# Performance work log

Hardware: AMD Instinct MI355X
Metric: run time of the kernel (lower is better)

Reference implementation:

```python
import jax, jax.numpy as jnp
import numpy as np
from jax import lax

NUM_TAGS = 9
HIDDEN = 768
BATCH = 64
SEQ = 512


def setup_inputs() -> dict:
    key = jax.random.key(0)
    ks = jax.random.split(key, 6)
    hidden = jax.random.normal(ks[0], (BATCH, SEQ, HIDDEN), dtype=jnp.float32)
    labels = jax.random.randint(ks[1], (BATCH, SEQ), 0, NUM_TAGS)  # all >= 0 -> full mask
    weight = jax.random.normal(ks[2], (NUM_TAGS, HIDDEN), dtype=jnp.float32) * 0.02
    bias = jnp.zeros((NUM_TAGS,), dtype=jnp.float32)
    start_transitions = jax.random.normal(ks[3], (NUM_TAGS,), dtype=jnp.float32) * 0.1
    end_transitions = jax.random.normal(ks[4], (NUM_TAGS,), dtype=jnp.float32) * 0.1
    transitions = jax.random.normal(ks[5], (NUM_TAGS, NUM_TAGS), dtype=jnp.float32) * 0.1
    return dict(hidden=hidden, labels=labels, weight=weight, bias=bias,
                start_transitions=start_transitions, end_transitions=end_transitions,
                transitions=transitions)


def _crf_log_likelihood(emissions, tags, mask, start_t, end_t, trans):
    """pytorch-crf log-likelihood, reduction='sum'.
    emissions [B,L,T] float, tags [B,L] int, mask [B,L] bool."""
    # --- numerator: score of the gold path ---
    tag0 = tags[:, 0]
    score0 = start_t[tag0] + jnp.take_along_axis(emissions[:, 0], tag0[:, None], axis=1)[:, 0]

    def num_step(carry, inp):
        score, prev = carry
        em, tg, m = inp  # em [B,T], tg [B], m [B]
        s = trans[prev, tg] + jnp.take_along_axis(em, tg[:, None], axis=1)[:, 0]
        score = score + jnp.where(m, s, jnp.zeros_like(s))
        prev = jnp.where(m, tg, prev)
        return (score, prev), None

    (num_score, last_tag), _ = lax.scan(
        num_step, (score0, tag0),
        (emissions[:, 1:].swapaxes(0, 1), tags[:, 1:].T, mask[:, 1:].T))
    numerator = num_score + end_t[last_tag]

    # --- denominator: forward algorithm (log-sum-exp recurrence) ---
    alpha0 = start_t[None, :] + emissions[:, 0]  # [B,T]

    def den_step(alpha, inp):
        em, m = inp  # em [B,T], m [B]
        nxt = jax.nn.logsumexp(alpha[:, :, None] + trans[None], axis=1) + em
        alpha = jnp.where(m[:, None], nxt, alpha)
        return alpha, None

    alpha, _ = lax.scan(den_step, alpha0,
                        (emissions[:, 1:].swapaxes(0, 1), mask[:, 1:].T))
    denominator = jax.nn.logsumexp(alpha + end_t[None, :], axis=1)

    return jnp.sum(numerator - denominator)


def _viterbi_decode(emissions, mask, start_t, end_t, trans):
    """Max-plus DP + backtrack. Returns padded [B,L] int32 best tag sequence."""
    B, L, T = emissions.shape
    score0 = start_t[None, :] + emissions[:, 0]  # [B,T]
    identity = jnp.arange(T, dtype=jnp.int32)[None, :]  # identity backpointer for masked steps

    def fwd_step(score, inp):
        em, m = inp  # em [B,T], m [B]
        br = score[:, :, None] + trans[None]  # [B,T_prev,T_cur]
        idx = jnp.argmax(br, axis=1).astype(jnp.int32)  # [B,T]
        nxt = jnp.max(br, axis=1) + em
        score = jnp.where(m[:, None], nxt, score)
        idx = jnp.where(m[:, None], idx, identity)
        return score, idx

    final, hist = lax.scan(fwd_step, score0,
                           (emissions[:, 1:].swapaxes(0, 1), mask[:, 1:].T))
    last_tag = jnp.argmax(final + end_t[None, :], axis=1).astype(jnp.int32)  # [B]

    def back_step(tag, idx):  # idx [B,T] backpointers for this position
        prev = jnp.take_along_axis(idx, tag[:, None], axis=1)[:, 0]
        return prev, tag

    first_tag, tags_rev = lax.scan(back_step, last_tag, hist, reverse=True)
    tags = jnp.concatenate([first_tag[None, :], tags_rev], axis=0).T  # [B,L]
    return tags * mask.astype(jnp.int32)


def reference(hidden, labels, weight, bias, start_transitions, end_transitions, transitions):
    mask_full = labels >= 0
    h = hidden[:, 1:-1, :]                       # drop [CLS]/[SEP] positions
    tags = labels[:, 1:-1] * mask_full[:, 1:-1]  # zero out padded labels
    mask = mask_full[:, 1:-1]
    # dropout is identity in eval mode
    emissions = jnp.einsum('blh,th->blt', h, weight) + bias  # [B,L,T]
    llh = _crf_log_likelihood(emissions, tags, mask,
                              start_transitions, end_transitions, transitions)
    tag_seqs = _viterbi_decode(emissions, mask,
                               start_transitions, end_transitions, transitions)
    return -llh, tag_seqs.astype(jnp.float32)
```

## Files before the change

kernel.cpp:

```cpp
#include <hip/hip_runtime.h>
#include <stdint.h>

#define NB 64
#define SEQL 512
#define L 510
#define T 9
#define H 768
#define EMS 12
#define LN2 0.6931471805599453f

__device__ __forceinline__ float rl(float v, int l) {
  return __uint_as_float(__builtin_amdgcn_readlane(__float_as_uint(v), l));
}

__global__ __launch_bounds__(256) void ka_kernel(
    const float* __restrict__ hidden, const float* __restrict__ weight,
    const float* __restrict__ bias, const float* __restrict__ trans,
    float* __restrict__ em, float* __restrict__ PdLn, float* __restrict__ Mv,
    float* __restrict__ out) {
  __shared__ float4 wl[1728];
  __shared__ float s_em[33 * 12];
  __shared__ float s_ee[33 * 12];
  const int tid = threadIdx.x;
  const int w = blockIdx.x;
  const int b = w >> 4, s = w & 15;
  const int nt = (s == 15) ? 29 : 32;
  const int l0 = 32 * s + 1;
  const int off0 = (s == 0) ? 1 : 0;
  const int nrows = nt + off0;
  const int lstart = l0 - off0;

  const float4* w4 = (const float4*)weight;
  for (int k = tid; k < 1728; k += 256) wl[k] = w4[k];
  if (w == 0 && tid == 0) out[0] = 0.f;
  __syncthreads();

  const int lane = tid & 63, wv = tid >> 6;
  float bs[9];
#pragma unroll
  for (int t = 0; t < 9; ++t) bs[t] = bias[t];

  for (int r = wv; r < nrows; r += 4) {
    const float4* h4 = (const float4*)(hidden + ((size_t)(b * SEQL + lstart + r + 1)) * H);
    float4 h0 = h4[lane], h1 = h4[lane + 64], h2 = h4[lane + 128];
    float acc[9];
#pragma unroll
    for (int t = 0; t < 9; ++t) acc[t] = 0.f;
#pragma unroll
    for (int t = 0; t < 9; ++t) {
      float4 wa = wl[t * 192 + lane];
      float4 wb = wl[t * 192 + lane + 64];
      float4 wc = wl[t * 192 + lane + 128];
      acc[t] = fmaf(h0.x, wa.x, fmaf(h0.y, wa.y, fmaf(h0.z, wa.z, fmaf(h0.w, wa.w, acc[t]))));
      acc[t] = fmaf(h1.x, wb.x, fmaf(h1.y, wb.y, fmaf(h1.z, wb.z, fmaf(h1.w, wb.w, acc[t]))));
      acc[t] = fmaf(h2.x, wc.x, fmaf(h2.y, wc.y, fmaf(h2.z, wc.z, fmaf(h2.w, wc.w, acc[t]))));
    }
#pragma unroll
    for (int off = 32; off; off >>= 1) {
#pragma unroll
      for (int t = 0; t < 9; ++t) acc[t] += __shfl_xor(acc[t], off);
    }
    if (lane == 0) {
      float* eo = em + ((size_t)(b * L + lstart + r)) * EMS;
#pragma unroll
      for (int t = 0; t < 9; ++t) {
        float v = acc[t] + bs[t];
        s_em[r * 12 + t] = v;
        s_ee[r * 12 + t] = __expf(v);
        eo[t] = v;
      }
    }
  }
  __syncthreads();

  if (tid < 64) {
    const int i9 = lane < 9 ? lane : 8;
    float E[81];
#pragma unroll
    for (int k = 0; k < 81; ++k) E[k] = __expf(trans[k]);
    const float* ee0 = s_ee + off0 * 12;
    float R[9];
#pragma unroll
    for (int j = 0; j < 9; ++j) R[j] = E[i9 * 9 + j] * ee0[j];
    int iexp = 0;
    for (int t = 1; t < nt; ++t) {
      const float* e = ee0 + t * 12;
      float4 ea = *(const float4*)e;
      float4 eb = *(const float4*)(e + 4);
      float e8 = e[8];
      float Rn[9];
#pragma unroll
      for (int j = 0; j < 9; ++j) {
        float a = R[0] * E[0 * 9 + j];
#pragma unroll
        for (int k = 1; k < 9; ++k) a = fmaf(R[k], E[k * 9 + j], a);
        Rn[j] = a;
      }
      R[0] = Rn[0] * ea.x; R[1] = Rn[1] * ea.y; R[2] = Rn[2] * ea.z;
      R[3] = Rn[3] * ea.w; R[4] = Rn[4] * eb.x; R[5] = Rn[5] * eb.y;
      R[6] = Rn[6] * eb.z; R[7] = Rn[7] * eb.w; R[8] = Rn[8] * e8;
      if ((t & 3) == 0) {
        float mx = R[0];
#pragma unroll
        for (int j = 1; j < 9; ++j) mx = fmaxf(mx, R[j]);
        int ex = (int)((__float_as_uint(mx) >> 23) & 0xff) - 127;
        iexp += ex;
        float sc = __uint_as_float((uint32_t)(127 - ex) << 23);
#pragma unroll
        for (int j = 0; j < 9; ++j) R[j] *= sc;
      }
    }
    if (lane < 9) {
      float ls = (float)iexp * LN2;
#pragma unroll
      for (int j = 0; j < 9; ++j)
        PdLn[(size_t)w * 81 + j * 9 + lane] = __logf(R[j]) + ls;
    }
  } else if (tid < 128) {
    const int i9 = lane < 9 ? lane : 8;
    float t_[81];
#pragma unroll
    for (int k = 0; k < 81; ++k) t_[k] = trans[k];
    const float* e0 = s_em + off0 * 12;
    float V[9];
#pragma unroll
    for (int j = 0; j < 9; ++j) V[j] = t_[i9 * 9 + j] + e0[j];
    for (int t = 1; t < nt; ++t) {
      const float* e = e0 + t * 12;
      float4 ea = *(const float4*)e;
      float4 eb = *(const float4*)(e + 4);
      float e8 = e[8];
      float ex[9] = {ea.x, ea.y, ea.z, ea.w, eb.x, eb.y, eb.z, eb.w, e8};
      float Vn[9];
#pragma unroll
      for (int j = 0; j < 9; ++j) {
        float m = V[0] + t_[0 * 9 + j];
#pragma unroll
        for (int k = 1; k < 9; ++k) m = fmaxf(m, V[k] + t_[k * 9 + j]);
        Vn[j] = m + ex[j];
      }
#pragma unroll
      for (int j = 0; j < 9; ++j) V[j] = Vn[j];
    }
    if (lane < 9) {
#pragma unroll
      for (int j = 0; j < 9; ++j)
        Mv[(size_t)w * 81 + j * 9 + lane] = V[j];
    }
  }
}

__global__ __launch_bounds__(256) void kb_kernel(
    const float* __restrict__ em, const int* __restrict__ labels,
    const float* __restrict__ PdLn, const float* __restrict__ Mv,
    const float* __restrict__ start_t, const float* __restrict__ end_t,
    const float* __restrict__ trans, float* __restrict__ out) {
  __shared__ float s_pd[1296];
  __shared__ float s_mv[1296];
  __shared__ float s_A[153];
  __shared__ float s_t[81];
  __shared__ float s_np[4];
  __shared__ int s_lab[L];
  __shared__ unsigned char s_ch[32];
  __shared__ uint32_t s_bp[32 * 16 * 2];
  const int b = blockIdx.x;
  const int tid = threadIdx.x;
  for (int k = tid; k < 1296; k += 256) {
    s_pd[k] = PdLn[(size_t)b * 1296 + k];
    s_mv[k] = Mv[(size_t)b * 1296 + k];
  }
  for (int k = tid; k < 81; k += 256) s_t[k] = trans[k];
  for (int k = tid; k < L; k += 256) s_lab[k] = labels[b * SEQL + 1 + k];
  __syncthreads();

  float part = 0.f;
  for (int l = tid; l < L; l += 256) {
    int tg = s_lab[l];
    float e = em[((size_t)(b * L + l)) * EMS + tg];
    if (l == 0) part += start_t[tg] + e;
    else part += s_t[s_lab[l - 1] * 9 + tg] + e;
    if (l == L - 1) part += end_t[tg];
  }
#pragma unroll
  for (int off = 32; off; off >>= 1) part += __shfl_xor(part, off);
  if ((tid & 63) == 0) s_np[tid >> 6] = part;
  __syncthreads();

  if (tid < 64) {
    const int lane = tid;
    const int jj = lane < 9 ? lane : 8;

    float D = start_t[jj] + em[(size_t)b * L * EMS + jj];
    for (int s = 0; s < 16; ++s) {
      const float* col = &s_pd[s * 81 + jj * 9];
      float v0 = rl(D, 0) + col[0], v1 = rl(D, 1) + col[1], v2 = rl(D, 2) + col[2];
      float v3 = rl(D, 3) + col[3], v4 = rl(D, 4) + col[4], v5 = rl(D, 5) + col[5];
      float v6 = rl(D, 6) + col[6], v7 = rl(D, 7) + col[7], v8 = rl(D, 8) + col[8];
      float mx = fmaxf(fmaxf(fmaxf(fmaxf(v0, v1), fmaxf(v2, v3)),
                             fmaxf(fmaxf(v4, v5), fmaxf(v6, v7))), v8);
      float sum = __expf(v0 - mx) + __expf(v1 - mx) + __expf(v2 - mx) +
                  __expf(v3 - mx) + __expf(v4 - mx) + __expf(v5 - mx) +
                  __expf(v6 - mx) + __expf(v7 - mx) + __expf(v8 - mx);
      D = mx + __logf(sum);
    }
    float fe = D + end_t[jj];
    float w0 = rl(fe, 0), w1 = rl(fe, 1), w2 = rl(fe, 2), w3 = rl(fe, 3);
    float w4 = rl(fe, 4), w5 = rl(fe, 5), w6 = rl(fe, 6), w7 = rl(fe, 7), w8 = rl(fe, 8);
    float mx = fmaxf(fmaxf(fmaxf(fmaxf(w0, w1), fmaxf(w2, w3)),
                           fmaxf(fmaxf(w4, w5), fmaxf(w6, w7))), w8);
    float den = mx + __logf(__expf(w0 - mx) + __expf(w1 - mx) + __expf(w2 - mx) +
                            __expf(w3 - mx) + __expf(w4 - mx) + __expf(w5 - mx) +
                            __expf(w6 - mx) + __expf(w7 - mx) + __expf(w8 - mx));
    if (lane == 0)
      atomicAdd(out, den - (s_np[0] + s_np[1] + s_np[2] + s_np[3]));

    float A = start_t[jj] + em[(size_t)b * L * EMS + jj];
    if (lane < 9) s_A[lane] = A;
    for (int s = 0; s < 16; ++s) {
      const float* col = &s_mv[s * 81 + jj * 9];
      float u0 = rl(A, 0) + col[0], u1 = rl(A, 1) + col[1], u2 = rl(A, 2) + col[2];
      float u3 = rl(A, 3) + col[3], u4 = rl(A, 4) + col[4], u5 = rl(A, 5) + col[5];
      float u6 = rl(A, 6) + col[6], u7 = rl(A, 7) + col[7], u8 = rl(A, 8) + col[8];
      A = fmaxf(fmaxf(fmaxf(fmaxf(u0, u1), fmaxf(u2, u3)),
                      fmaxf(fmaxf(u4, u5), fmaxf(u6, u7))), u8);
      if (lane < 9) s_A[(s + 1) * 9 + lane] = A;
    }
    float fv = A + end_t[jj];
    int j = 0;
    {
      float bv = rl(fv, 0);
#pragma unroll
      for (int i = 1; i < 9; ++i) { float v = rl(fv, i); if (v > bv) { bv = v; j = i; } }
    }
    for (int s = 15; s >= 0; --s) {
      float val = s_A[s * 9 + jj] + s_mv[s * 81 + j * 9 + jj];
      int ii = 0;
      float bb = rl(val, 0);
#pragma unroll
      for (int i = 1; i < 9; ++i) { float v = rl(val, i); if (v > bb) { bb = v; ii = i; } }
      if (lane == 0) {
        s_ch[s * 2] = (unsigned char)ii;
        s_ch[s * 2 + 1] = (unsigned char)j;
      }
      j = ii;
    }
    if (lane == 0) out[1 + (size_t)b * L] = (float)j;
  }
  __syncthreads();

  if (tid < 16) {
    const int s = tid;
    const int nt = (s == 15) ? 29 : 32;
    const int l0 = 32 * s + 1;
    const int i0 = s_ch[s * 2];
    const int jF = s_ch[s * 2 + 1];
    float t_[81];
#pragma unroll
    for (int k = 0; k < 81; ++k) t_[k] = trans[k];
    const float* ep = em + ((size_t)(b * L + l0)) * EMS;
    float a[9];
    {
      float4 ea = *(const float4*)(ep);
      float4 eb = *(const float4*)(ep + 4);
      float e8 = ep[8];
      float e[9] = {ea.x, ea.y, ea.z, ea.w, eb.x, eb.y, eb.z, eb.w, e8};
#pragma unroll
      for (int jx = 0; jx < 9; ++jx) a[jx] = t_[i0 * 9 + jx] + e[jx];
    }
    for (int q = 1; q < nt; ++q) {
      float4 na = *(const float4*)(ep + (size_t)q * EMS);
      float4 nb = *(const float4*)(ep + (size_t)q * EMS + 4);
      float n8 = ep[(size_t)q * EMS + 8];
      float e[9] = {na.x, na.y, na.z, na.w, nb.x, nb.y, nb.z, nb.w, n8};
      uint32_t pk0 = 0, pk1 = 0;
      float an[9];
#pragma unroll
      for (int jx = 0; jx < 9; ++jx) {
        float best = a[0] + t_[0 * 9 + jx];
        int bi = 0;
#pragma unroll
        for (int k = 1; k < 9; ++k) {
          float v = a[k] + t_[k * 9 + jx];
          if (v > best) { best = v; bi = k; }
        }
        an[jx] = best + e[jx];
        if (jx < 8) pk0 |= ((uint32_t)bi) << (4 * jx);
        else pk1 = (uint32_t)bi;
      }
      s_bp[(q * 16 + s) * 2] = pk0;
      s_bp[(q * 16 + s) * 2 + 1] = pk1;
#pragma unroll
      for (int jx = 0; jx < 9; ++jx) a[jx] = an[jx];
    }
    int cur = jF;
    float* orow = out + 1 + (size_t)b * L + l0;
    for (int q = nt - 1; q >= 1; --q) {
      orow[q] = (float)cur;
      uint32_t pk = s_bp[(q * 16 + s) * 2 + (cur >> 3)];
      cur = (int)((pk >> ((cur & 7) * 4)) & 15u);
    }
    orow[0] = (float)cur;
  }
}

extern "C" void kernel_launch(void* const* d_in, const int* in_sizes, int n_in,
                              void* d_out, int out_size, void* d_ws, size_t ws_size,
                              hipStream_t stream) {
  const float* hidden  = (const float*)d_in[0];
  const int*   labels  = (const int*)d_in[1];
  const float* weight  = (const float*)d_in[2];
  const float* bias    = (const float*)d_in[3];
  const float* start_t = (const float*)d_in[4];
  const float* end_t   = (const float*)d_in[5];
  const float* trans   = (const float*)d_in[6];
  float* out = (float*)d_out;

  float* em   = (float*)d_ws;
  float* PdLn = em + (size_t)NB * L * EMS;
  float* Mv   = PdLn + (size_t)1024 * 81;

  ka_kernel<<<1024, 256, 0, stream>>>(hidden, weight, bias, trans, em, PdLn, Mv, out);
  kb_kernel<<<NB, 256, 0, stream>>>(em, labels, PdLn, Mv, start_t, end_t, trans, out);
}
```

Measured before the change: 248.1 us.

## Split emission GEMV into its own kernel and move segment CRF scans into kb

The first kernel now only computes emissions, two rows per wave, and prefetches the next pair of hidden rows while the current pair is being reduced. The per-segment forward (sum-product) and max-product 32-step scans move into the per-batch kernel. There they run from shared-memory staged emissions, four segments per wave. This is meant to stop 1024 blocks from stalling on serial scan latency behind their bandwidth-bound loads, and it removes the PdLn/Mv global round trip. The cost is fewer blocks doing the serial scans, exp recomputation inside the scan, and more shared memory in kb.

```diff
diff --git a/kernel.cpp b/kernel.cpp
--- a/kernel.cpp
+++ b/kernel.cpp
@@ -7,154 +7,90 @@
 #define T 9
 #define H 768
 #define EMS 12
+#define WST 388
 #define LN2 0.6931471805599453f
 
 __device__ __forceinline__ float rl(float v, int l) {
   return __uint_as_float(__builtin_amdgcn_readlane(__float_as_uint(v), l));
 }
 
-__global__ __launch_bounds__(256) void ka_kernel(
+__global__ __launch_bounds__(256) void emis_kernel(
     const float* __restrict__ hidden, const float* __restrict__ weight,
-    const float* __restrict__ bias, const float* __restrict__ trans,
-    float* __restrict__ em, float* __restrict__ PdLn, float* __restrict__ Mv,
+    const float* __restrict__ bias, float* __restrict__ em,
     float* __restrict__ out) {
   __shared__ float4 wl[1728];
-  __shared__ float s_em[33 * 12];
-  __shared__ float s_ee[33 * 12];
-  const int tid = threadIdx.x;
-  const int w = blockIdx.x;
-  const int b = w >> 4, s = w & 15;
-  const int nt = (s == 15) ? 29 : 32;
-  const int l0 = 32 * s + 1;
-  const int off0 = (s == 0) ? 1 : 0;
-  const int nrows = nt + off0;
-  const int lstart = l0 - off0;
-
   const float4* w4 = (const float4*)weight;
-  for (int k = tid; k < 1728; k += 256) wl[k] = w4[k];
-  if (w == 0 && tid == 0) out[0] = 0.f;
+  for (int k = threadIdx.x; k < 1728; k += 256) wl[k] = w4[k];
+  if (blockIdx.x == 0 && threadIdx.x == 0) out[0] = 0.f;
   __syncthreads();
-
-  const int lane = tid & 63, wv = tid >> 6;
-  float bs[9];
-#pragma unroll
-  for (int t = 0; t < 9; ++t) bs[t] = bias[t];
-
-  for (int r = wv; r < nrows; r += 4) {
-    const float4* h4 = (const float4*)(hidden + ((size_t)(b * SEQL + lstart + r + 1)) * H);
-    float4 h0 = h4[lane], h1 = h4[lane + 64], h2 = h4[lane + 128];
-    float acc[9];
-#pragma unroll
-    for (int t = 0; t < 9; ++t) acc[t] = 0.f;
-#pragma unroll
-    for (int t = 0; t < 9; ++t) {
-      float4 wa = wl[t * 192 + lane];
-      float4 wb = wl[t * 192 + lane + 64];
-      float4 wc = wl[t * 192 + lane + 128];
-      acc[t] = fmaf(h0.x, wa.x, fmaf(h0.y, wa.y, fmaf(h0.z, wa.z, fmaf(h0.w, wa.w, acc[t]))));
-      acc[t] = fmaf(h1.x, wb.x, fmaf(h1.y, wb.y, fmaf(h1.z, wb.z, fmaf(h1.w, wb.w, acc[t]))));
-      acc[t] = fmaf(h2.x, wc.x, fmaf(h2.y, wc.y, fmaf(h2.z, wc.z, fmaf(h2.w, wc.w, acc[t]))));
+  const int lane = threadIdx.x & 63;
+  const int wv = threadIdx.x >> 6;
+  const int base = blockIdx.x * 32 + wv * 8;
+  const float bj = bias[lane < 9 ? lane : 0];
+
+  float4 ha[3], hb[3];
+  {
+    const int r0 = base, r1 = base + 1;
+    const int b0 = r0 / L, p0 = r0 - b0 * L;
+    const int b1 = r1 / L, p1 = r1 - b1 * L;
+    const float4* h0 = (const float4*)(hidden + ((size_t)(b0 * SEQL + p0 + 1)) * H);
+    const float4* h1 = (const float4*)(hidden + ((size_t)(b1 * SEQL + p1 + 1)) * H);
+#pragma unroll
+    for (int k = 0; k < 3; ++k) { ha[k] = h0[lane + 64 * k]; hb[k] = h1[lane + 64 * k]; }
+  }
+#pragma unroll 1
+  for (int pr = 0; pr < 4; ++pr) {
+    const int r0 = base + pr * 2, r1 = r0 + 1;
+    float4 na[3], nb[3];
+    if (pr < 3) {
+      const int q0 = r0 + 2, q1 = r0 + 3;
+      const int c0 = q0 / L, s0 = q0 - c0 * L;
+      const int c1 = q1 / L, s1 = q1 - c1 * L;
+      const float4* h0 = (const float4*)(hidden + ((size_t)(c0 * SEQL + s0 + 1)) * H);
+      const float4* h1 = (const float4*)(hidden + ((size_t)(c1 * SEQL + s1 + 1)) * H);
+#pragma unroll
+      for (int k = 0; k < 3; ++k) { na[k] = h0[lane + 64 * k]; nb[k] = h1[lane + 64 * k]; }
+    }
+    float a0[T], a1[T];
+#pragma unroll
+    for (int t = 0; t < T; ++t) { a0[t] = 0.f; a1[t] = 0.f; }
+#pragma unroll
+    for (int t = 0; t < T; ++t) {
+#pragma unroll
+      for (int k = 0; k < 3; ++k) {
+        float4 w = wl[t * 192 + lane + 64 * k];
+        a0[t] = fmaf(ha[k].x, w.x, fmaf(ha[k].y, w.y, fmaf(ha[k].z, w.z, fmaf(ha[k].w, w.w, a0[t]))));
+        a1[t] = fmaf(hb[k].x, w.x, fmaf(hb[k].y, w.y, fmaf(hb[k].z, w.z, fmaf(hb[k].w, w.w, a1[t]))));
+      }
     }
 #pragma unroll
     for (int off = 32; off; off >>= 1) {
 #pragma unroll
-      for (int t = 0; t < 9; ++t) acc[t] += __shfl_xor(acc[t], off);
-    }
-    if (lane == 0) {
-      float* eo = em + ((size_t)(b * L + lstart + r)) * EMS;
-#pragma unroll
-      for (int t = 0; t < 9; ++t) {
-        float v = acc[t] + bs[t];
-        s_em[r * 12 + t] = v;
-        s_ee[r * 12 + t] = __expf(v);
-        eo[t] = v;
-      }
-    }
-  }
-  __syncthreads();
-
-  if (tid < 64) {
-    const int i9 = lane < 9 ? lane : 8;
-    float E[81];
-#pragma unroll
-    for (int k = 0; k < 81; ++k) E[k] = __expf(trans[k]);
-    const float* ee0 = s_ee + off0 * 12;
-    float R[9];
-#pragma unroll
-    for (int j = 0; j < 9; ++j) R[j] = E[i9 * 9 + j] * ee0[j];
-    int iexp = 0;
-    for (int t = 1; t < nt; ++t) {
-      const float* e = ee0 + t * 12;
-      float4 ea = *(const float4*)e;
-      float4 eb = *(const float4*)(e + 4);
-      float e8 = e[8];
-      float Rn[9];
-#pragma unroll
-      for (int j = 0; j < 9; ++j) {
-        float a = R[0] * E[0 * 9 + j];
-#pragma unroll
-        for (int k = 1; k < 9; ++k) a = fmaf(R[k], E[k * 9 + j], a);
-        Rn[j] = a;
-      }
-      R[0] = Rn[0] * ea.x; R[1] = Rn[1] * ea.y; R[2] = Rn[2] * ea.z;
-      R[3] = Rn[3] * ea.w; R[4] = Rn[4] * eb.x; R[5] = Rn[5] * eb.y;
-      R[6] = Rn[6] * eb.z; R[7] = Rn[7] * eb.w; R[8] = Rn[8] * e8;
-      if ((t & 3) == 0) {
-        float mx = R[0];
-#pragma unroll
-        for (int j = 1; j < 9; ++j) mx = fmaxf(mx, R[j]);
-        int ex = (int)((__float_as_uint(mx) >> 23) & 0xff) - 127;
-        iexp += ex;
-        float sc = __uint_as_float((uint32_t)(127 - ex) << 23);
-#pragma unroll
-        for (int j = 0; j < 9; ++j) R[j] *= sc;
-      }
+      for (int t = 0; t < T; ++t) {
+        a0[t] += __shfl_xor(a0[t], off);
+        a1[t] += __shfl_xor(a1[t], off);
+      }
+    }
+    float v0 = a0[0], v1 = a1[0];
+#pragma unroll
+    for (int t = 1; t < T; ++t) {
+      v0 = (lane == t) ? a0[t] : v0;
+      v1 = (lane == t) ? a1[t] : v1;
     }
     if (lane < 9) {
-      float ls = (float)iexp * LN2;
-#pragma unroll
-      for (int j = 0; j < 9; ++j)
-        PdLn[(size_t)w * 81 + j * 9 + lane] = __logf(R[j]) + ls;
-    }
-  } else if (tid < 128) {
-    const int i9 = lane < 9 ? lane : 8;
-    float t_[81];
-#pragma unroll
-    for (int k = 0; k < 81; ++k) t_[k] = trans[k];
-    const float* e0 = s_em + off0 * 12;
-    float V[9];
-#pragma unroll
-    for (int j = 0; j < 9; ++j) V[j] = t_[i9 * 9 + j] + e0[j];
-    for (int t = 1; t < nt; ++t) {
-      const float* e = e0 + t * 12;
-      float4 ea = *(const float4*)e;
-      float4 eb = *(const float4*)(e + 4);
-      float e8 = e[8];
-      float ex[9] = {ea.x, ea.y, ea.z, ea.w, eb.x, eb.y, eb.z, eb.w, e8};
-      float Vn[9];
-#pragma unroll
-      for (int j = 0; j < 9; ++j) {
-        float m = V[0] + t_[0 * 9 + j];
-#pragma unroll
-        for (int k = 1; k < 9; ++k) m = fmaxf(m, V[k] + t_[k * 9 + j]);
-        Vn[j] = m + ex[j];
-      }
-#pragma unroll
-      for (int j = 0; j < 9; ++j) V[j] = Vn[j];
-    }
-    if (lane < 9) {
-#pragma unroll
-      for (int j = 0; j < 9; ++j)
-        Mv[(size_t)w * 81 + j * 9 + lane] = V[j];
-    }
+      em[(size_t)r0 * EMS + lane] = v0 + bj;
+      em[(size_t)r1 * EMS + lane] = v1 + bj;
+    }
+#pragma unroll
+    for (int k = 0; k < 3; ++k) { ha[k] = na[k]; hb[k] = nb[k]; }
   }
 }
 
 __global__ __launch_bounds__(256) void kb_kernel(
     const float* __restrict__ em, const int* __restrict__ labels,
-    const float* __restrict__ PdLn, const float* __restrict__ Mv,
     const float* __restrict__ start_t, const float* __restrict__ end_t,
     const float* __restrict__ trans, float* __restrict__ out) {
+  __shared__ float s_emb[16 * WST];
   __shared__ float s_pd[1296];
   __shared__ float s_mv[1296];
   __shared__ float s_A[153];
@@ -165,12 +101,18 @@
   __shared__ uint32_t s_bp[32 * 16 * 2];
   const int b = blockIdx.x;
   const int tid = threadIdx.x;
-  for (int k = tid; k < 1296; k += 256) {
-    s_pd[k] = PdLn[(size_t)b * 1296 + k];
-    s_mv[k] = Mv[(size_t)b * 1296 + k];
-  }
+
   for (int k = tid; k < 81; k += 256) s_t[k] = trans[k];
   for (int k = tid; k < L; k += 256) s_lab[k] = labels[b * SEQL + 1 + k];
+  for (int idx = tid; idx < 16 * 32 * 3; idx += 256) {
+    const int s = idx / 96, rem = idx - 96 * s;
+    const int r = rem / 3, c = rem - 3 * r;
+    const int row = 32 * s + 1 + r;
+    if (row < L) {
+      float4 v = *(const float4*)(em + ((size_t)(b * L + row)) * EMS + c * 4);
+      *(float4*)(s_emb + s * WST + r * 12 + c * 4) = v;
+    }
+  }
   __syncthreads();
 
   float part = 0.f;
@@ -184,12 +126,80 @@
 #pragma unroll
   for (int off = 32; off; off >>= 1) part += __shfl_xor(part, off);
   if ((tid & 63) == 0) s_np[tid >> 6] = part;
+
+  const int lane = tid & 63, wv = tid >> 6;
+  const int g = lane / 9;
+  const int i9 = lane - g * 9;
+  const bool act = g < 4;
+  const int sw = wv * 4 + (act ? g : 0);
+  const int ntw = (sw == 15) ? 29 : 32;
+  const float* ew = s_emb + sw * WST;
+
+  {
+    float E[81];
+#pragma unroll
+    for (int k = 0; k < 81; ++k) E[k] = __expf(trans[k]);
+    float R[9];
+#pragma unroll
+    for (int j = 0; j < 9; ++j) R[j] = E[i9 * 9 + j] * __expf(ew[j]);
+    int iexp = 0;
+    for (int t = 1; t < ntw; ++t) {
+      float e[9];
+#pragma unroll
+      for (int j = 0; j < 9; ++j) e[j] = __expf(ew[t * 12 + j]);
+      float Rn[9];
+#pragma unroll
+      for (int j = 0; j < 9; ++j) {
+        float a = R[0] * E[0 * 9 + j];
+#pragma unroll
+        for (int k = 1; k < 9; ++k) a = fmaf(R[k], E[k * 9 + j], a);
+        Rn[j] = a;
+      }
+#pragma unroll
+      for (int j = 0; j < 9; ++j) R[j] = Rn[j] * e[j];
+      if ((t & 3) == 0) {
+        float mx = R[0];
+#pragma unroll
+        for (int j = 1; j < 9; ++j) mx = fmaxf(mx, R[j]);
+        int ex = (int)((__float_as_uint(mx) >> 23) & 0xff) - 127;
+        iexp += ex;
+        float sc = __uint_as_float((uint32_t)(127 - ex) << 23);
+#pragma unroll
+        for (int j = 0; j < 9; ++j) R[j] *= sc;
+      }
+    }
+    if (act) {
+      float ls = (float)iexp * LN2;
+#pragma unroll
+      for (int j = 0; j < 9; ++j)
+        s_pd[sw * 81 + j * 9 + i9] = __logf(R[j]) + ls;
+    }
+  }
+  {
+    float V[9];
+#pragma unroll
+    for (int j = 0; j < 9; ++j) V[j] = trans[i9 * 9 + j] + ew[j];
+    for (int t = 1; t < ntw; ++t) {
+      float Vn[9];
+#pragma unroll
+      for (int j = 0; j < 9; ++j) {
+        float m = V[0] + trans[0 * 9 + j];
+#pragma unroll
+        for (int k = 1; k < 9; ++k) m = fmaxf(m, V[k] + trans[k * 9 + j]);
+        Vn[j] = m + ew[t * 12 + j];
+      }
+#pragma unroll
+      for (int j = 0; j < 9; ++j) V[j] = Vn[j];
+    }
+    if (act) {
+#pragma unroll
+      for (int j = 0; j < 9; ++j) s_mv[sw * 81 + j * 9 + i9] = V[j];
+    }
+  }
   __syncthreads();
 
   if (tid < 64) {
-    const int lane = tid;
     const int jj = lane < 9 ? lane : 8;
-
     float D = start_t[jj] + em[(size_t)b * L * EMS + jj];
     for (int s = 0; s < 16; ++s) {
       const float* col = &s_pd[s * 81 + jj * 9];
@@ -254,36 +264,23 @@
     const int l0 = 32 * s + 1;
     const int i0 = s_ch[s * 2];
     const int jF = s_ch[s * 2 + 1];
-    float t_[81];
-#pragma unroll
-    for (int k = 0; k < 81; ++k) t_[k] = trans[k];
-    const float* ep = em + ((size_t)(b * L + l0)) * EMS;
+    const float* ep = s_emb + s * WST;
     float a[9];
-    {
-      float4 ea = *(const float4*)(ep);
-      float4 eb = *(const float4*)(ep + 4);
-      float e8 = ep[8];
-      float e[9] = {ea.x, ea.y, ea.z, ea.w, eb.x, eb.y, eb.z, eb.w, e8};
-#pragma unroll
-      for (int jx = 0; jx < 9; ++jx) a[jx] = t_[i0 * 9 + jx] + e[jx];
-    }
+#pragma unroll
+    for (int jx = 0; jx < 9; ++jx) a[jx] = trans[i0 * 9 + jx] + ep[jx];
     for (int q = 1; q < nt; ++q) {
-      float4 na = *(const float4*)(ep + (size_t)q * EMS);
-      float4 nb = *(const float4*)(ep + (size_t)q * EMS + 4);
-      float n8 = ep[(size_t)q * EMS + 8];
-      float e[9] = {na.x, na.y, na.z, na.w, nb.x, nb.y, nb.z, nb.w, n8};
       uint32_t pk0 = 0, pk1 = 0;
       float an[9];
 #pragma unroll
       for (int jx = 0; jx < 9; ++jx) {
-        float best = a[0] + t_[0 * 9 + jx];
+        float best = a[0] + trans[0 * 9 + jx];
         int bi = 0;
 #pragma unroll
         for (int k = 1; k < 9; ++k) {
-          float v = a[k] + t_[k * 9 + jx];
+          float v = a[k] + trans[k * 9 + jx];
           if (v > best) { best = v; bi = k; }
         }
-        an[jx] = best + e[jx];
+        an[jx] = best + ep[q * 12 + jx];
         if (jx < 8) pk0 |= ((uint32_t)bi) << (4 * jx);
         else pk1 = (uint32_t)bi;
       }
@@ -315,10 +312,8 @@
   const float* trans   = (const float*)d_in[6];
   float* out = (float*)d_out;
 
-  float* em   = (float*)d_ws;
-  float* PdLn = em + (size_t)NB * L * EMS;
-  float* Mv   = PdLn + (size_t)1024 * 81;
-
-  ka_kernel<<<1024, 256, 0, stream>>>(hidden, weight, bias, trans, em, PdLn, Mv, out);
-  kb_kernel<<<NB, 256, 0, stream>>>(em, labels, PdLn, Mv, start_t, end_t, trans, out);
+  float* em = (float*)d_ws;
+
+  emis_kernel<<<1020, 256, 0, stream>>>(hidden, weight, bias, em, out);
+  kb_kernel<<<NB, 256, 0, stream>>>(em, labels, start_t, end_t, trans, out);
 }
```

Result: faster. 233.6 us (-5.9%).
